# Kernel tuning notes

Measured on AMD Instinct MI355X. Metric: run time of the kernel, lower is better.

The kernel has to match this reference:

```python
import jax, jax.numpy as jnp
import numpy as np

D_MODEL = 1024
N_HEADS = 8
EDGE_HID = 512
N_EDGE_CLS = 18
N_NODE_CLS = 18
MAX_NODES = 15


def setup_inputs() -> dict:
    key = jax.random.key(0)
    ks = jax.random.split(key, 24)
    B, T, L, D = 32, 4, 1024, D_MODEL
    N = MAX_NODES
    s = 0.02
    visual_feats = jax.random.normal(ks[0], (B, T, L, D), jnp.float32)
    nodes = jax.random.randint(ks[1], (B, N), 0, N_NODE_CLS, dtype=jnp.int32)
    bboxes = jax.random.uniform(ks[2], (B, N, 4), jnp.float32)
    # embedding table; padding_idx=-1 -> last row zeroed (unused due to clamp)
    emb = (jax.random.normal(ks[3], (N_NODE_CLS + 1, D)) * s).at[-1].set(0.0)
    Wb = jax.random.normal(ks[4], (D, 4)) * s
    bb = jnp.zeros((D,), jnp.float32)
    Wq = jax.random.normal(ks[5], (D, D)) * s
    bq = jnp.zeros((D,), jnp.float32)
    Wk = jax.random.normal(ks[6], (D, D)) * s
    bk = jnp.zeros((D,), jnp.float32)
    Wv = jax.random.normal(ks[7], (D, D)) * s
    bv = jnp.zeros((D,), jnp.float32)
    Wo = jax.random.normal(ks[8], (D, D)) * s
    bo = jnp.zeros((D,), jnp.float32)
    W1 = jax.random.normal(ks[9], (EDGE_HID, 2 * D)) * s
    b1 = jnp.zeros((EDGE_HID,), jnp.float32)
    W2 = jax.random.normal(ks[10], (N_EDGE_CLS, EDGE_HID)) * s
    b2 = jnp.zeros((N_EDGE_CLS,), jnp.float32)
    Wh1 = jax.random.normal(ks[11], (256, D)) * s
    bh1 = jnp.zeros((256,), jnp.float32)
    Wh2 = jax.random.normal(ks[12], (1, 256)) * s
    bh2 = jnp.zeros((1,), jnp.float32)
    return dict(visual_feats=visual_feats, nodes=nodes, bboxes=bboxes, emb=emb,
                Wb=Wb, bb=bb, Wq=Wq, bq=bq, Wk=Wk, bk=bk, Wv=Wv, bv=bv,
                Wo=Wo, bo=bo, W1=W1, b1=b1, W2=W2, b2=b2,
                Wh1=Wh1, bh1=bh1, Wh2=Wh2, bh2=bh2)


def reference(visual_feats, nodes, bboxes, emb, Wb, bb, Wq, bq, Wk, bk, Wv, bv,
              Wo, bo, W1, b1, W2, b2, Wh1, bh1, Wh2, bh2):
    B, T, L, D = visual_feats.shape
    H = N_HEADS
    Hd = D // H
    v_f = visual_feats[:, -1]  # (B, L, D)
    n_emb = emb[jnp.maximum(nodes, 0)]            # (B, N, D)
    query = n_emb + bboxes @ Wb.T + bb            # (B, N, D)
    N = query.shape[1]
    # multi-head cross-attention (query=nodes, key/value=visual tokens)
    q = (query @ Wq.T + bq).reshape(B, N, H, Hd)
    k = (v_f @ Wk.T + bk).reshape(B, L, H, Hd)
    v = (v_f @ Wv.T + bv).reshape(B, L, H, Hd)
    scores = jnp.einsum('bnhd,blhd->bhnl', q, k) / jnp.sqrt(jnp.float32(Hd))
    attn = jax.nn.softmax(scores, axis=-1)
    ctx = jnp.einsum('bhnl,blhd->bnhd', attn, v).reshape(B, N, D)
    enriched = ctx @ Wo.T + bo                    # (B, N, D)
    pad = nodes == -1                             # all False here
    clean = jnp.where(pad[..., None], 0.0, enriched)
    # edge MLP: decompose first Linear over the concat into two half matmuls
    h_i = enriched @ W1[:, :D].T                  # (B, N, E)
    h_j = enriched @ W1[:, D:].T                  # (B, N, E)
    pair = jax.nn.relu(h_i[:, :, None, :] + h_j[:, None, :, :] + b1)  # (B,N,N,E)
    edge_logits = pair @ W2.T + b2                # (B, N, N, 18)
    valid = jnp.maximum(jnp.sum(~pad, axis=1, keepdims=True), 1).astype(enriched.dtype)
    gfeat = jnp.sum(clean, axis=1) / valid        # (B, D)
    energy = (jax.nn.relu(gfeat @ Wh1.T + bh1) @ Wh2.T + bh2).squeeze(-1)  # (B,)
    return edge_logits, energy
```

## Files before the change

### kernel.cpp

```cpp
#include <hip/hip_runtime.h>


typedef __attribute__((ext_vector_type(8))) short bf16x8;
typedef __attribute__((ext_vector_type(4))) float f32x4;

__device__ __forceinline__ unsigned short f2bf(float f) {
    unsigned int u = __float_as_uint(f);
    u = u + 0x7FFFu + ((u >> 16) & 1u);
    return (unsigned short)(u >> 16);
}

__device__ __forceinline__ void gload_lds16(const void* g, void* l) {
    __builtin_amdgcn_global_load_lds(
        (const __attribute__((address_space(1))) void*)g,
        (__attribute__((address_space(3))) void*)l,
        16, 0, 0);
}

__global__ __launch_bounds__(256) void bfgemm_k(
    const unsigned short* __restrict__ A, const unsigned short* __restrict__ B,
    unsigned short* __restrict__ C, int M, long sA, long sB, long sC)
{
    const int b  = blockIdx.z;
    const int m0 = blockIdx.y * 64;
    const int n0 = blockIdx.x * 128;
    const unsigned short* Ab = A + b * sA;
    const unsigned short* Bb = B + b * sB;

    __shared__ __align__(16) unsigned short As[64 * 32];
    __shared__ __align__(16) unsigned short Bs[128 * 32];

    const int t    = threadIdx.x;
    const int lane = t & 63;
    const int w    = t >> 6;
    const int wm   = w >> 1, wn = w & 1;

    f32x4 acc[2][4] = {};

    const int ar = t >> 2;
    const int ac = (t & 3) * 8;

    unsigned short* AsW  = As + w * 512;
    unsigned short* BsW0 = Bs + w * 512;
    unsigned short* BsW1 = Bs + 2048 + w * 512;
    const unsigned short* ga  = Ab + (long)(m0 + ar) * 1024 + ac;
    const unsigned short* gb0 = Bb + (long)(n0 + ar) * 1024 + ac;
    const unsigned short* gb1 = Bb + (long)(n0 + 64 + ar) * 1024 + ac;

    for (int k0 = 0; k0 < 1024; k0 += 32) {
        __syncthreads();
        gload_lds16(ga  + k0, AsW);
        gload_lds16(gb0 + k0, BsW0);
        gload_lds16(gb1 + k0, BsW1);
        __syncthreads();

        const int krow = (lane >> 4) * 8;
        bf16x8 af[2], bf[4];
#pragma unroll
        for (int fi = 0; fi < 2; ++fi)
            af[fi] = *(const bf16x8*)&As[(wm * 32 + fi * 16 + (lane & 15)) * 32 + krow];
#pragma unroll
        for (int fj = 0; fj < 4; ++fj)
            bf[fj] = *(const bf16x8*)&Bs[(wn * 64 + fj * 16 + (lane & 15)) * 32 + krow];
#pragma unroll
        for (int fi = 0; fi < 2; ++fi)
#pragma unroll
            for (int fj = 0; fj < 4; ++fj)
                acc[fi][fj] = __builtin_amdgcn_mfma_f32_16x16x32_bf16(
                    af[fi], bf[fj], acc[fi][fj], 0, 0, 0);
    }

    const int rbase = (lane >> 4) * 4;
    const int cn    = n0 + wn * 64 + (lane & 15);
#pragma unroll
    for (int fi = 0; fi < 2; ++fi) {
        const int mb = m0 + wm * 32 + fi * 16 + rbase;
#pragma unroll
        for (int r = 0; r < 4; ++r) {
            const int m = mb + r;
            if (m < M) {
#pragma unroll
                for (int fj = 0; fj < 4; ++fj)
                    C[b * sC + (long)m * 1024 + cn + fj * 16] = f2bf(acc[fi][fj][r]);
            }
        }
    }
}

__global__ __launch_bounds__(256) void sgemm_k(
    const unsigned short* __restrict__ A, const float* __restrict__ Bf,
    float* __restrict__ C, int M, long sA, long sB, long sC)
{
    const int b  = blockIdx.z;
    const int m0 = blockIdx.y * 64;
    const int n0 = blockIdx.x * 128;
    const unsigned short* Ab = A + b * sA;
    const float* Bb = Bf + b * sB;
    float* Cb = C + b * sC;

    __shared__ __align__(16) unsigned short As[64 * 32];
    __shared__ __align__(16) unsigned short Bs[128 * 32];

    const int t    = threadIdx.x;
    const int lane = t & 63;
    const int w    = t >> 6;
    const int wm   = w >> 1, wn = w & 1;

    f32x4 acc[2][4] = {};

    const int ar = t >> 2;
    const int ac = (t & 3) * 8;

    unsigned short* AsW = As + w * 512;
    const unsigned short* ga = Ab + (long)(m0 + ar) * 1024 + ac;
    const float* gb0 = Bb + (long)(n0 + ar) * 1024 + ac;
    const float* gb1 = Bb + (long)(n0 + 64 + ar) * 1024 + ac;

    for (int k0 = 0; k0 < 1024; k0 += 32) {
        float4 v0a = *(const float4*)(gb0 + k0);
        float4 v0b = *(const float4*)(gb0 + k0 + 4);
        float4 v1a = *(const float4*)(gb1 + k0);
        float4 v1b = *(const float4*)(gb1 + k0 + 4);
        __syncthreads();
        gload_lds16(ga + k0, AsW);
        ushort4 o;
        o.x = f2bf(v0a.x); o.y = f2bf(v0a.y); o.z = f2bf(v0a.z); o.w = f2bf(v0a.w);
        *(ushort4*)&Bs[t * 8] = o;
        o.x = f2bf(v0b.x); o.y = f2bf(v0b.y); o.z = f2bf(v0b.z); o.w = f2bf(v0b.w);
        *(ushort4*)&Bs[t * 8 + 4] = o;
        o.x = f2bf(v1a.x); o.y = f2bf(v1a.y); o.z = f2bf(v1a.z); o.w = f2bf(v1a.w);
        *(ushort4*)&Bs[2048 + t * 8] = o;
        o.x = f2bf(v1b.x); o.y = f2bf(v1b.y); o.z = f2bf(v1b.z); o.w = f2bf(v1b.w);
        *(ushort4*)&Bs[2048 + t * 8 + 4] = o;
        __syncthreads();

        const int krow = (lane >> 4) * 8;
        bf16x8 af[2], bf[4];
#pragma unroll
        for (int fi = 0; fi < 2; ++fi)
            af[fi] = *(const bf16x8*)&As[(wm * 32 + fi * 16 + (lane & 15)) * 32 + krow];
#pragma unroll
        for (int fj = 0; fj < 4; ++fj)
            bf[fj] = *(const bf16x8*)&Bs[(wn * 64 + fj * 16 + (lane & 15)) * 32 + krow];
#pragma unroll
        for (int fi = 0; fi < 2; ++fi)
#pragma unroll
            for (int fj = 0; fj < 4; ++fj)
                acc[fi][fj] = __builtin_amdgcn_mfma_f32_16x16x32_bf16(
                    af[fi], bf[fj], acc[fi][fj], 0, 0, 0);
    }

    const int rbase = (lane >> 4) * 4;
    const int cn    = n0 + wn * 64 + (lane & 15);
#pragma unroll
    for (int fi = 0; fi < 2; ++fi) {
        const int mb = m0 + wm * 32 + fi * 16 + rbase;
#pragma unroll
        for (int r = 0; r < 4; ++r) {
            const int m = mb + r;
            if (m < M) {
#pragma unroll
                for (int fj = 0; fj < 4; ++fj)
                    Cb[(long)m * 1024 + cn + fj * 16] = acc[fi][fj][r];
            }
        }
    }
}

template <int OM>
__global__ __launch_bounds__(256) void pgemm_k(
    const unsigned short* __restrict__ A, const unsigned short* __restrict__ B,
    const float* __restrict__ bias, float* __restrict__ C,
    unsigned short* __restrict__ Cbf,
    int M, int K, int lda, int ldb, int ldc)
{
    const int m0 = blockIdx.y * 64;
    const int n0 = blockIdx.x * 64;

    __shared__ __align__(16) unsigned short As[64 * 32];
    __shared__ __align__(16) unsigned short Bs[64 * 32];

    const int t    = threadIdx.x;
    const int lane = t & 63;
    const int w    = t >> 6;
    const int wm   = w >> 1, wn = w & 1;
    const int lm   = lane & 15, lg = lane >> 4;

    const int ar = t >> 2;
    const int ac = (t & 3) * 8;

    f32x4 acc[2][2] = {};

    unsigned short* AsW = As + w * 512;
    unsigned short* BsW = Bs + w * 512;
    const unsigned short* ga = A + (long)(m0 + ar) * lda + ac;
    const unsigned short* gb = B + (long)(n0 + ar) * ldb + ac;

    for (int k0 = 0; k0 < K; k0 += 32) {
        __syncthreads();
        gload_lds16(ga + k0, AsW);
        gload_lds16(gb + k0, BsW);
        __syncthreads();

        const int krow = lg * 8 & 24;
        bf16x8 af[2], bf[2];
#pragma unroll
        for (int fi = 0; fi < 2; ++fi)
            af[fi] = *(const bf16x8*)&As[(wm * 32 + fi * 16 + lm) * 32 + krow];
#pragma unroll
        for (int fj = 0; fj < 2; ++fj)
            bf[fj] = *(const bf16x8*)&Bs[(wn * 32 + fj * 16 + lm) * 32 + krow];
#pragma unroll
        for (int fi = 0; fi < 2; ++fi)
#pragma unroll
            for (int fj = 0; fj < 2; ++fj)
                acc[fi][fj] = __builtin_amdgcn_mfma_f32_16x16x32_bf16(
                    af[fi], bf[fj], acc[fi][fj], 0, 0, 0);
    }

    const int rbase = lg * 4;
#pragma unroll
    for (int fi = 0; fi < 2; ++fi) {
        const int mb = m0 + wm * 32 + fi * 16 + rbase;
#pragma unroll
        for (int r = 0; r < 4; ++r) {
            const int m = mb + r;
            if (m < M) {
#pragma unroll
                for (int fj = 0; fj < 2; ++fj) {
                    const int n = n0 + wn * 32 + fj * 16 + lm;
                    float v = acc[fi][fj][r];
                    if (bias) v += bias[n];
                    if constexpr (OM != 2) C[(long)m * ldc + n] = v;
                    if constexpr (OM >= 1) Cbf[(long)m * ldc + n] = f2bf(v);
                }
            }
        }
    }
}

__global__ __launch_bounds__(256) void qw_k(
    const unsigned short* __restrict__ qbf, const unsigned short* __restrict__ WkT,
    unsigned short* __restrict__ qW, float scale)
{
    const int z = blockIdx.y;
    const int b = z >> 3, h = z & 7;
    const int w = threadIdx.x >> 6, lane = threadIdx.x & 63;
    const int lm = lane & 15, lg = lane >> 4;
    const int n0w = blockIdx.x * 256 + w * 64;

    const unsigned short* Ar = qbf + (long)(b * 15 + lm) * 1024 + h * 128 + lg * 8;
    const unsigned short* Br = WkT + (long)(n0w + lm) * 1024 + h * 128 + lg * 8;

    bf16x8 af[4];
#pragma unroll
    for (int ks = 0; ks < 4; ++ks) af[ks] = *(const bf16x8*)(Ar + ks * 32);

    f32x4 acc[4] = {};
#pragma unroll
    for (int fj = 0; fj < 4; ++fj) {
#pragma unroll
        for (int ks = 0; ks < 4; ++ks) {
            bf16x8 bf = *(const bf16x8*)(Br + (long)fj * 16 * 1024 + ks * 32);
            acc[fj] = __builtin_amdgcn_mfma_f32_16x16x32_bf16(af[ks], bf, acc[fj], 0, 0, 0);
        }
    }

#pragma unroll
    for (int r = 0; r < 4; ++r) {
        const int m = lg * 4 + r;
        if (m < 15) {
#pragma unroll
            for (int fj = 0; fj < 4; ++fj)
                qW[(long)b * 131072 + (long)(m * 8 + h) * 1024 + n0w + fj * 16 + lm]
                    = f2bf(acc[fj][r] * scale);
        }
    }
}

__global__ __launch_bounds__(256) void ctx_k(
    const unsigned short* __restrict__ cf, const unsigned short* __restrict__ Wvb,
    const float* __restrict__ bv, unsigned short* __restrict__ ctx)
{
    const int z = blockIdx.x;
    const int b = z >> 3, h = z & 7;
    const int w = threadIdx.x >> 6, lane = threadIdx.x & 63;
    const int lm = lane & 15, lg = lane >> 4;

    const unsigned short* Ar = cf + (long)b * 122880 + (long)(lm * 8 + h) * 1024 + lg * 8;
    const unsigned short* Br = Wvb + (long)(h * 128 + w * 32 + lm) * 1024 + lg * 8;

    f32x4 acc[2] = {};
    for (int k0 = 0; k0 < 1024; k0 += 32) {
        bf16x8 af = *(const bf16x8*)(Ar + k0);
        bf16x8 b0 = *(const bf16x8*)(Br + k0);
        bf16x8 b1 = *(const bf16x8*)(Br + 16 * 1024 + k0);
        acc[0] = __builtin_amdgcn_mfma_f32_16x16x32_bf16(af, b0, acc[0], 0, 0, 0);
        acc[1] = __builtin_amdgcn_mfma_f32_16x16x32_bf16(af, b1, acc[1], 0, 0, 0);
    }

#pragma unroll
    for (int r = 0; r < 4; ++r) {
        const int m = lg * 4 + r;
        if (m < 15) {
#pragma unroll
            for (int fj = 0; fj < 2; ++fj) {
                const int gcol = h * 128 + w * 32 + fj * 16 + lm;
                ctx[(long)(b * 15 + m) * 1024 + gcol] = f2bf(acc[fj][r] + bv[gcol]);
            }
        }
    }
}

__global__ __launch_bounds__(256) void uber_cvt_k(
    const int* __restrict__ nodes, const float* __restrict__ bboxes,
    const float* __restrict__ emb, const float* __restrict__ Wb,
    const float* __restrict__ bb, unsigned short* __restrict__ qbf,
    const float* __restrict__ Wq, const float* __restrict__ Wo,
    const float* __restrict__ Wv, const float* __restrict__ W1,
    const float* __restrict__ Wk,
    unsigned short* __restrict__ dWq, unsigned short* __restrict__ dWo,
    unsigned short* __restrict__ dWv, unsigned short* __restrict__ dW1r,
    unsigned short* __restrict__ dWkT)
{
    __shared__ unsigned short tile[64][72];
    const int bid = blockIdx.x;
    const int t = threadIdx.x;

    if (bid < 4096) {
        const int which = bid >> 10;
        const int i = (bid & 1023) * 256 + t;
        const float* s;
        unsigned short* d;
        if (which == 3) {
            const int flat = i * 4, n = flat >> 10, k = flat & 1023;
            s = (n < 512) ? W1 + (long)n * 2048 + k
                          : W1 + (long)(n - 512) * 2048 + 1024 + k;
            d = dW1r + flat;
        } else {
            s = (which == 0 ? Wq : which == 1 ? Wo : Wv) + (long)i * 4;
            d = (which == 0 ? dWq : which == 1 ? dWo : dWv) + (long)i * 4;
        }
        float4 v = *(const float4*)s;
        ushort4 o;
        o.x = f2bf(v.x); o.y = f2bf(v.y); o.z = f2bf(v.z); o.w = f2bf(v.w);
        *(ushort4*)d = o;
    } else if (bid < 4352) {
        const int tl = bid - 4096;
        const int d0 = (tl >> 4) * 64, e0 = (tl & 15) * 64;
        const int r0 = t >> 4, c0 = (t & 15) * 4;
#pragma unroll
        for (int rr = 0; rr < 4; ++rr) {
            const int r = r0 + rr * 16;
            float4 v = *(const float4*)&Wk[(long)(d0 + r) * 1024 + e0 + c0];
            tile[r][c0 + 0] = f2bf(v.x); tile[r][c0 + 1] = f2bf(v.y);
            tile[r][c0 + 2] = f2bf(v.z); tile[r][c0 + 3] = f2bf(v.w);
        }
        __syncthreads();
#pragma unroll
        for (int rr = 0; rr < 4; ++rr) {
            const int idx = rr * 256 + t;
            const int e = idx >> 4, c4 = (idx & 15) * 4;
            ushort4 o;
            o.x = tile[c4 + 0][e]; o.y = tile[c4 + 1][e];
            o.z = tile[c4 + 2][e]; o.w = tile[c4 + 3][e];
            *(ushort4*)&dWkT[(long)(e0 + e) * 1024 + d0 + c4] = o;
        }
    } else {
        const int blk = bid - 4352;
        const int node = nodes[blk];
        const int idx = node < 0 ? 0 : node;
        const float4 bx = *(const float4*)&bboxes[blk * 4];
        const float* er = emb + (long)idx * 1024;
        for (int d = t; d < 1024; d += 256) {
            const float4 w = *(const float4*)&Wb[d * 4];
            qbf[(long)blk * 1024 + d] = f2bf(
                er[d] + bb[d] + bx.x * w.x + bx.y * w.y + bx.z * w.z + bx.w * w.w);
        }
    }
}

__global__ __launch_bounds__(256) void cvtT_k(
    const float* __restrict__ vf, unsigned short* __restrict__ vbfT)
{
    const int b  = blockIdx.z;
    const int e0 = blockIdx.x * 64;
    const int l0 = blockIdx.y * 64;
    const float* src = vf + (long)b * 4194304;
    __shared__ unsigned short tile[64][72];
    const int t = threadIdx.x;
    const int r0 = t >> 4, c0 = (t & 15) * 4;
#pragma unroll
    for (int rr = 0; rr < 4; ++rr) {
        const int r = r0 + rr * 16;
        float4 v = *(const float4*)&src[(long)(l0 + r) * 1024 + e0 + c0];
        tile[r][c0 + 0] = f2bf(v.x); tile[r][c0 + 1] = f2bf(v.y);
        tile[r][c0 + 2] = f2bf(v.z); tile[r][c0 + 3] = f2bf(v.w);
    }
    __syncthreads();
#pragma unroll
    for (int rr = 0; rr < 4; ++rr) {
        const int idx = rr * 256 + t;
        const int e   = idx >> 4;
        const int c4  = (idx & 15) * 4;
        ushort4 o;
        o.x = tile[c4 + 0][e]; o.y = tile[c4 + 1][e];
        o.z = tile[c4 + 2][e]; o.w = tile[c4 + 3][e];
        *(ushort4*)&vbfT[(long)b * 1048576 + (long)(e0 + e) * 1024 + l0 + c4] = o;
    }
}

__global__ __launch_bounds__(256) void softmax_k(
    const float* __restrict__ sc, unsigned short* __restrict__ attn)
{
    __shared__ float red[4];
    const int blk = blockIdx.x;
    const int b = blk / 120, r = blk % 120;
    const float* p = sc + (long)blk * 1024;
    const int t = threadIdx.x;
    float4 v = *(const float4*)&p[t * 4];

    float m = fmaxf(fmaxf(v.x, v.y), fmaxf(v.z, v.w));
#pragma unroll
    for (int o = 32; o; o >>= 1) m = fmaxf(m, __shfl_xor(m, o));
    if ((t & 63) == 0) red[t >> 6] = m;
    __syncthreads();
    m = fmaxf(fmaxf(red[0], red[1]), fmaxf(red[2], red[3]));
    __syncthreads();

    v.x = __expf(v.x - m); v.y = __expf(v.y - m);
    v.z = __expf(v.z - m); v.w = __expf(v.w - m);
    float s = v.x + v.y + v.z + v.w;
#pragma unroll
    for (int o = 32; o; o >>= 1) s += __shfl_xor(s, o);
    if ((t & 63) == 0) red[t >> 6] = s;
    __syncthreads();
    s = red[0] + red[1] + red[2] + red[3];
    const float inv = 1.0f / s;
    ushort4 o;
    o.x = f2bf(v.x * inv); o.y = f2bf(v.y * inv);
    o.z = f2bf(v.z * inv); o.w = f2bf(v.w * inv);
    *(ushort4*)&attn[(long)(b * 128 + r) * 1024 + t * 4] = o;
}

__global__ __launch_bounds__(320) void tail_k(
    const float* __restrict__ hh, const float* __restrict__ b1,
    const float* __restrict__ W2, const float* __restrict__ b2,
    const float* __restrict__ enr, const int* __restrict__ nodes,
    const float* __restrict__ Wh1, const float* __restrict__ bh1,
    const float* __restrict__ Wh2, float* __restrict__ hidr,
    float* __restrict__ out)
{
    __shared__ float sm[8993];
    const int bid = blockIdx.x;
    const int t = threadIdx.x;

    if (bid < 480) {
        const int b = bid / 15, i = bid % 15;
        float* hiS = sm;
        float* b1S = sm + 256;
        float* hjS = sm + 512;
        float* w2S = sm + 512 + 3855;
        const int j = t / 18, c = t % 18;
        float acc = 0.0f;

        for (int u0 = 0; u0 < 512; u0 += 256) {
            __syncthreads();
            if (t < 64) {
                float4 v = *(const float4*)&hh[(long)(b * 15 + i) * 1024 + u0 + t * 4];
                hiS[t * 4 + 0] = v.x; hiS[t * 4 + 1] = v.y;
                hiS[t * 4 + 2] = v.z; hiS[t * 4 + 3] = v.w;
            } else if (t < 128) {
                const int tt = t - 64;
                float4 v = *(const float4*)&b1[u0 + tt * 4];
                b1S[tt * 4 + 0] = v.x; b1S[tt * 4 + 1] = v.y;
                b1S[tt * 4 + 2] = v.z; b1S[tt * 4 + 3] = v.w;
            }
            for (int x = t; x < 960; x += 320) {
                const int r = x >> 6, cc = (x & 63) * 4;
                float4 v = *(const float4*)&hh[(long)(b * 15 + r) * 1024 + 512 + u0 + cc];
                hjS[r * 257 + cc + 0] = v.x; hjS[r * 257 + cc + 1] = v.y;
                hjS[r * 257 + cc + 2] = v.z; hjS[r * 257 + cc + 3] = v.w;
            }
            for (int x = t; x < 1152; x += 320) {
                const int r = x >> 6, cc = (x & 63) * 4;
                float4 v = *(const float4*)&W2[(long)r * 512 + u0 + cc];
                w2S[r * 257 + cc + 0] = v.x; w2S[r * 257 + cc + 1] = v.y;
                w2S[r * 257 + cc + 2] = v.z; w2S[r * 257 + cc + 3] = v.w;
            }
            __syncthreads();
            if (t < 270) {
                for (int u = 0; u < 256; ++u) {
                    float p = hiS[u] + hjS[j * 257 + u] + b1S[u];
                    p = p > 0.0f ? p : 0.0f;
                    acc += p * w2S[c * 257 + u];
                }
            }
        }
        if (t < 270)
            out[((long)(bid) * 15 + j) * 18 + c] = acc + b2[c];
    } else {
        const int z = bid - 480;
        const int u0 = (z & 15) * 16;
        const int b  = z >> 4;
        float* gf = sm;

        int cnt = 0;
#pragma unroll
        for (int n = 0; n < 15; ++n) cnt += (nodes[b * 15 + n] != -1) ? 1 : 0;
        const float inv_valid = 1.0f / fmaxf((float)cnt, 1.0f);
        if (t < 256) {
            for (int e = t; e < 1024; e += 256) {
                float s = 0.0f;
#pragma unroll
                for (int n = 0; n < 15; ++n) {
                    const bool ok = nodes[b * 15 + n] != -1;
                    s += ok ? enr[(long)(b * 15 + n) * 1024 + e] : 0.0f;
                }
                gf[e] = s * inv_valid;
            }
        }
        __syncthreads();
        if (t < 256) {
            const int wave = t >> 6, lane = t & 63;
#pragma unroll
            for (int r = 0; r < 4; ++r) {
                const int u = u0 + wave * 4 + r;
                float s = 0.0f;
#pragma unroll
                for (int e0 = 0; e0 < 1024; e0 += 64)
                    s += gf[e0 + lane] * Wh1[(long)u * 1024 + e0 + lane];
#pragma unroll
                for (int o = 32; o; o >>= 1) s += __shfl_xor(s, o);
                if (lane == 0)
                    hidr[b * 256 + u] = fmaxf(s + bh1[u], 0.0f) * Wh2[u];
            }
        }
    }
}

__global__ __launch_bounds__(256) void energy3_k(
    const float* __restrict__ hidr, const float* __restrict__ bh2,
    float* __restrict__ out)
{
    const int b = blockIdx.x;
    const int t = threadIdx.x;
    __shared__ float red[4];
    float v = hidr[b * 256 + t];
#pragma unroll
    for (int o = 32; o; o >>= 1) v += __shfl_xor(v, o);
    if ((t & 63) == 0) red[t >> 6] = v;
    __syncthreads();
    if (t == 0) out[129600 + b] = red[0] + red[1] + red[2] + red[3] + bh2[0];
}

extern "C" void kernel_launch(void* const* d_in, const int* in_sizes, int n_in,
                              void* d_out, int out_size, void* d_ws, size_t ws_size,
                              hipStream_t stream)
{
    const float* visual = (const float*)d_in[0];
    const int*   nodes  = (const int*)  d_in[1];
    const float* bboxes = (const float*)d_in[2];
    const float* emb    = (const float*)d_in[3];
    const float* Wb     = (const float*)d_in[4];
    const float* bb     = (const float*)d_in[5];
    const float* Wq     = (const float*)d_in[6];
    const float* bq     = (const float*)d_in[7];
    const float* Wk     = (const float*)d_in[8];
    const float* Wv     = (const float*)d_in[10];
    const float* bv     = (const float*)d_in[11];
    const float* Wo     = (const float*)d_in[12];
    const float* bo     = (const float*)d_in[13];
    const float* W1     = (const float*)d_in[14];
    const float* b1     = (const float*)d_in[15];
    const float* W2     = (const float*)d_in[16];
    const float* b2     = (const float*)d_in[17];
    const float* Wh1    = (const float*)d_in[18];
    const float* bh1    = (const float*)d_in[19];
    const float* Wh2    = (const float*)d_in[20];
    const float* bh2    = (const float*)d_in[21];

    float* out = (float*)d_out;
    float* ws  = (float*)d_ws;

    unsigned short* query_bf = (unsigned short*)(ws);
    unsigned short* q_bf     = (unsigned short*)(ws + 131072);
    float* scores = ws + 262144;
    unsigned short* ctxf_bf  = (unsigned short*)(ws + 4194304);
    unsigned short* ctx_bf   = (unsigned short*)(ws + 6160384);
    float* enr    = ws + 6422528;
    unsigned short* enr_bf   = (unsigned short*)(ws + 6914048);
    float* hh     = ws + 7176192;
    unsigned short* Wq_bf  = (unsigned short*)(ws + 7667712);
    unsigned short* Wo_bf  = (unsigned short*)(ws + 8192000);
    unsigned short* Wv_bf  = (unsigned short*)(ws + 8716288);
    unsigned short* W1r_bf = (unsigned short*)(ws + 9240576);
    unsigned short* WkT_bf = (unsigned short*)(ws + 9764864);
    unsigned short* qW_bf   = (unsigned short*)(ws + 10289152);
    unsigned short* attn_bf = (unsigned short*)(ws + 12386304);
    unsigned short* v_bfT   = (unsigned short*)(ws + 31260672);
    float* hidr   = ws + 48070656;

    const float inv_sqrt_hd = 0.08838834764831845f;
    const float* v_f = visual + 3 * 1048576;

    uber_cvt_k<<<4832, 256, 0, stream>>>(
        nodes, bboxes, emb, Wb, bb, query_bf,
        Wq, Wo, Wv, W1, Wk, Wq_bf, Wo_bf, Wv_bf, W1r_bf, WkT_bf);

    pgemm_k<2><<<dim3(16, 8), 256, 0, stream>>>(
        query_bf, Wq_bf, bq, nullptr, q_bf, 480, 1024, 1024, 1024, 1024);

    qw_k<<<dim3(4, 256), 256, 0, stream>>>(q_bf, WkT_bf, qW_bf, inv_sqrt_hd);

    sgemm_k<<<dim3(8, 2, 32), 256, 0, stream>>>(
        qW_bf, v_f, scores, 120, 131072, 4194304, 122880);

    cvtT_k<<<dim3(16, 16, 32), 256, 0, stream>>>(v_f, v_bfT);

    softmax_k<<<3840, 256, 0, stream>>>(scores, attn_bf);

    bfgemm_k<<<dim3(8, 2, 32), 256, 0, stream>>>(
        attn_bf, v_bfT, ctxf_bf, 120, 131072, 1048576, 122880);

    ctx_k<<<256, 256, 0, stream>>>(ctxf_bf, Wv_bf, bv, ctx_bf);

    pgemm_k<1><<<dim3(16, 8), 256, 0, stream>>>(
        ctx_bf, Wo_bf, bo, enr, enr_bf, 480, 1024, 1024, 1024, 1024);

    pgemm_k<0><<<dim3(16, 8), 256, 0, stream>>>(
        enr_bf, W1r_bf, nullptr, hh, nullptr, 480, 1024, 1024, 1024, 1024);

    tail_k<<<992, 320, 0, stream>>>(
        hh, b1, W2, b2, enr, nodes, Wh1, bh1, Wh2, hidr, out);

    energy3_k<<<32, 256, 0, stream>>>(hidr, bh2, out);
}
```

Before: 215.9 us.

## Merge score GEMM with V transpose-convert, fold energy reduction into tail

The scores GEMM (sgemm) and the bf16 transpose-conversion of the visual features (cvtT) now run as a single launch, with blocks split by block index and sharing one LDS buffer. The energy head is moved into tail_k: each of 32 blocks computes all 256 hidden units and the final reduction, which removes the energy3 launch and the hidr workspace round trip. Together this drops two kernel launches and lets the two independent reads of v_f overlap. The cost is that the energy part now has only 32 blocks each doing 16x the work serially, where there were 512 blocks before, which could lengthen the tail kernel's critical path.

```diff
diff --git a/kernel.cpp b/kernel.cpp
--- a/kernel.cpp
+++ b/kernel.cpp
@@ -87,82 +87,113 @@
     }
 }
 
-__global__ __launch_bounds__(256) void sgemm_k(
-    const unsigned short* __restrict__ A, const float* __restrict__ Bf,
-    float* __restrict__ C, int M, long sA, long sB, long sC)
-{
-    const int b  = blockIdx.z;
-    const int m0 = blockIdx.y * 64;
-    const int n0 = blockIdx.x * 128;
-    const unsigned short* Ab = A + b * sA;
-    const float* Bb = Bf + b * sB;
-    float* Cb = C + b * sC;
-
-    __shared__ __align__(16) unsigned short As[64 * 32];
-    __shared__ __align__(16) unsigned short Bs[128 * 32];
-
-    const int t    = threadIdx.x;
-    const int lane = t & 63;
-    const int w    = t >> 6;
-    const int wm   = w >> 1, wn = w & 1;
-
-    f32x4 acc[2][4] = {};
-
-    const int ar = t >> 2;
-    const int ac = (t & 3) * 8;
-
-    unsigned short* AsW = As + w * 512;
-    const unsigned short* ga = Ab + (long)(m0 + ar) * 1024 + ac;
-    const float* gb0 = Bb + (long)(n0 + ar) * 1024 + ac;
-    const float* gb1 = Bb + (long)(n0 + 64 + ar) * 1024 + ac;
-
-    for (int k0 = 0; k0 < 1024; k0 += 32) {
-        float4 v0a = *(const float4*)(gb0 + k0);
-        float4 v0b = *(const float4*)(gb0 + k0 + 4);
-        float4 v1a = *(const float4*)(gb1 + k0);
-        float4 v1b = *(const float4*)(gb1 + k0 + 4);
-        __syncthreads();
-        gload_lds16(ga + k0, AsW);
-        ushort4 o;
-        o.x = f2bf(v0a.x); o.y = f2bf(v0a.y); o.z = f2bf(v0a.z); o.w = f2bf(v0a.w);
-        *(ushort4*)&Bs[t * 8] = o;
-        o.x = f2bf(v0b.x); o.y = f2bf(v0b.y); o.z = f2bf(v0b.z); o.w = f2bf(v0b.w);
-        *(ushort4*)&Bs[t * 8 + 4] = o;
-        o.x = f2bf(v1a.x); o.y = f2bf(v1a.y); o.z = f2bf(v1a.z); o.w = f2bf(v1a.w);
-        *(ushort4*)&Bs[2048 + t * 8] = o;
-        o.x = f2bf(v1b.x); o.y = f2bf(v1b.y); o.z = f2bf(v1b.z); o.w = f2bf(v1b.w);
-        *(ushort4*)&Bs[2048 + t * 8 + 4] = o;
-        __syncthreads();
-
-        const int krow = (lane >> 4) * 8;
-        bf16x8 af[2], bf[4];
-#pragma unroll
-        for (int fi = 0; fi < 2; ++fi)
-            af[fi] = *(const bf16x8*)&As[(wm * 32 + fi * 16 + (lane & 15)) * 32 + krow];
-#pragma unroll
-        for (int fj = 0; fj < 4; ++fj)
-            bf[fj] = *(const bf16x8*)&Bs[(wn * 64 + fj * 16 + (lane & 15)) * 32 + krow];
-#pragma unroll
-        for (int fi = 0; fi < 2; ++fi)
+__global__ __launch_bounds__(256) void sv_k(
+    const unsigned short* __restrict__ A, const float* __restrict__ vf,
+    float* __restrict__ C, unsigned short* __restrict__ vbfT, int M)
+{
+    __shared__ __align__(16) unsigned short sm_u[6144];
+    const int bid = blockIdx.x;
+    const int t = threadIdx.x;
+
+    if (bid < 512) {
+        const int b  = bid >> 4;
+        const int m0 = ((bid >> 3) & 1) * 64;
+        const int n0 = (bid & 7) * 128;
+        const unsigned short* Ab = A + (long)b * 131072;
+        const float* Bb = vf + (long)b * 4194304;
+        float* Cb = C + (long)b * 122880;
+
+        unsigned short* As = sm_u;
+        unsigned short* Bs = sm_u + 2048;
+
+        const int lane = t & 63;
+        const int w    = t >> 6;
+        const int wm   = w >> 1, wn = w & 1;
+
+        f32x4 acc[2][4] = {};
+
+        const int ar = t >> 2;
+        const int ac = (t & 3) * 8;
+
+        unsigned short* AsW = As + w * 512;
+        const unsigned short* ga = Ab + (long)(m0 + ar) * 1024 + ac;
+        const float* gb0 = Bb + (long)(n0 + ar) * 1024 + ac;
+        const float* gb1 = Bb + (long)(n0 + 64 + ar) * 1024 + ac;
+
+        for (int k0 = 0; k0 < 1024; k0 += 32) {
+            float4 v0a = *(const float4*)(gb0 + k0);
+            float4 v0b = *(const float4*)(gb0 + k0 + 4);
+            float4 v1a = *(const float4*)(gb1 + k0);
+            float4 v1b = *(const float4*)(gb1 + k0 + 4);
+            __syncthreads();
+            gload_lds16(ga + k0, AsW);
+            ushort4 o;
+            o.x = f2bf(v0a.x); o.y = f2bf(v0a.y); o.z = f2bf(v0a.z); o.w = f2bf(v0a.w);
+            *(ushort4*)&Bs[t * 8] = o;
+            o.x = f2bf(v0b.x); o.y = f2bf(v0b.y); o.z = f2bf(v0b.z); o.w = f2bf(v0b.w);
+            *(ushort4*)&Bs[t * 8 + 4] = o;
+            o.x = f2bf(v1a.x); o.y = f2bf(v1a.y); o.z = f2bf(v1a.z); o.w = f2bf(v1a.w);
+            *(ushort4*)&Bs[2048 + t * 8] = o;
+            o.x = f2bf(v1b.x); o.y = f2bf(v1b.y); o.z = f2bf(v1b.z); o.w = f2bf(v1b.w);
+            *(ushort4*)&Bs[2048 + t * 8 + 4] = o;
+            __syncthreads();
+
+            const int krow = (lane >> 4) * 8;
+            bf16x8 af[2], bf[4];
+#pragma unroll
+            for (int fi = 0; fi < 2; ++fi)
+                af[fi] = *(const bf16x8*)&As[(wm * 32 + fi * 16 + (lane & 15)) * 32 + krow];
 #pragma unroll
             for (int fj = 0; fj < 4; ++fj)
-                acc[fi][fj] = __builtin_amdgcn_mfma_f32_16x16x32_bf16(
-                    af[fi], bf[fj], acc[fi][fj], 0, 0, 0);
-    }
-
-    const int rbase = (lane >> 4) * 4;
-    const int cn    = n0 + wn * 64 + (lane & 15);
-#pragma unroll
-    for (int fi = 0; fi < 2; ++fi) {
-        const int mb = m0 + wm * 32 + fi * 16 + rbase;
-#pragma unroll
-        for (int r = 0; r < 4; ++r) {
-            const int m = mb + r;
-            if (m < M) {
+                bf[fj] = *(const bf16x8*)&Bs[(wn * 64 + fj * 16 + (lane & 15)) * 32 + krow];
+#pragma unroll
+            for (int fi = 0; fi < 2; ++fi)
 #pragma unroll
                 for (int fj = 0; fj < 4; ++fj)
-                    Cb[(long)m * 1024 + cn + fj * 16] = acc[fi][fj][r];
-            }
+                    acc[fi][fj] = __builtin_amdgcn_mfma_f32_16x16x32_bf16(
+                        af[fi], bf[fj], acc[fi][fj], 0, 0, 0);
+        }
+
+        const int rbase = (lane >> 4) * 4;
+        const int cn    = n0 + wn * 64 + (lane & 15);
+#pragma unroll
+        for (int fi = 0; fi < 2; ++fi) {
+            const int mb = m0 + wm * 32 + fi * 16 + rbase;
+#pragma unroll
+            for (int r = 0; r < 4; ++r) {
+                const int m = mb + r;
+                if (m < M) {
+#pragma unroll
+                    for (int fj = 0; fj < 4; ++fj)
+                        Cb[(long)m * 1024 + cn + fj * 16] = acc[fi][fj][r];
+                }
+            }
+        }
+    } else {
+        const int tl = bid - 512;
+        const int b  = tl >> 8;
+        const int e0 = (tl & 15) * 64;
+        const int l0 = ((tl >> 4) & 15) * 64;
+        const float* src = vf + (long)b * 4194304;
+        unsigned short* tile = sm_u;
+        const int r0 = t >> 4, c0 = (t & 15) * 4;
+#pragma unroll
+        for (int rr = 0; rr < 4; ++rr) {
+            const int r = r0 + rr * 16;
+            float4 v = *(const float4*)&src[(long)(l0 + r) * 1024 + e0 + c0];
+            tile[r * 72 + c0 + 0] = f2bf(v.x); tile[r * 72 + c0 + 1] = f2bf(v.y);
+            tile[r * 72 + c0 + 2] = f2bf(v.z); tile[r * 72 + c0 + 3] = f2bf(v.w);
+        }
+        __syncthreads();
+#pragma unroll
+        for (int rr = 0; rr < 4; ++rr) {
+            const int idx = rr * 256 + t;
+            const int e   = idx >> 4;
+            const int c4  = (idx & 15) * 4;
+            ushort4 o;
+            o.x = tile[(c4 + 0) * 72 + e]; o.y = tile[(c4 + 1) * 72 + e];
+            o.z = tile[(c4 + 2) * 72 + e]; o.w = tile[(c4 + 3) * 72 + e];
+            *(ushort4*)&vbfT[(long)b * 1048576 + (long)(e0 + e) * 1024 + l0 + c4] = o;
         }
     }
 }
@@ -380,36 +411,6 @@
     }
 }
 
-__global__ __launch_bounds__(256) void cvtT_k(
-    const float* __restrict__ vf, unsigned short* __restrict__ vbfT)
-{
-    const int b  = blockIdx.z;
-    const int e0 = blockIdx.x * 64;
-    const int l0 = blockIdx.y * 64;
-    const float* src = vf + (long)b * 4194304;
-    __shared__ unsigned short tile[64][72];
-    const int t = threadIdx.x;
-    const int r0 = t >> 4, c0 = (t & 15) * 4;
-#pragma unroll
-    for (int rr = 0; rr < 4; ++rr) {
-        const int r = r0 + rr * 16;
-        float4 v = *(const float4*)&src[(long)(l0 + r) * 1024 + e0 + c0];
-        tile[r][c0 + 0] = f2bf(v.x); tile[r][c0 + 1] = f2bf(v.y);
-        tile[r][c0 + 2] = f2bf(v.z); tile[r][c0 + 3] = f2bf(v.w);
-    }
-    __syncthreads();
-#pragma unroll
-    for (int rr = 0; rr < 4; ++rr) {
-        const int idx = rr * 256 + t;
-        const int e   = idx >> 4;
-        const int c4  = (idx & 15) * 4;
-        ushort4 o;
-        o.x = tile[c4 + 0][e]; o.y = tile[c4 + 1][e];
-        o.z = tile[c4 + 2][e]; o.w = tile[c4 + 3][e];
-        *(ushort4*)&vbfT[(long)b * 1048576 + (long)(e0 + e) * 1024 + l0 + c4] = o;
-    }
-}
-
 __global__ __launch_bounds__(256) void softmax_k(
     const float* __restrict__ sc, unsigned short* __restrict__ attn)
 {
@@ -448,7 +449,7 @@
     const float* __restrict__ W2, const float* __restrict__ b2,
     const float* __restrict__ enr, const int* __restrict__ nodes,
     const float* __restrict__ Wh1, const float* __restrict__ bh1,
-    const float* __restrict__ Wh2, float* __restrict__ hidr,
+    const float* __restrict__ Wh2, const float* __restrict__ bh2,
     float* __restrict__ out)
 {
     __shared__ float sm[8993];
@@ -500,10 +501,10 @@
         if (t < 270)
             out[((long)(bid) * 15 + j) * 18 + c] = acc + b2[c];
     } else {
-        const int z = bid - 480;
-        const int u0 = (z & 15) * 16;
-        const int b  = z >> 4;
-        float* gf = sm;
+        const int b = bid - 480;
+        float* gf  = sm;
+        float* hid = sm + 1024;
+        float* red = sm + 1280;
 
         int cnt = 0;
 #pragma unroll
@@ -523,35 +524,31 @@
         __syncthreads();
         if (t < 256) {
             const int wave = t >> 6, lane = t & 63;
-#pragma unroll
-            for (int r = 0; r < 4; ++r) {
-                const int u = u0 + wave * 4 + r;
-                float s = 0.0f;
-#pragma unroll
-                for (int e0 = 0; e0 < 1024; e0 += 64)
-                    s += gf[e0 + lane] * Wh1[(long)u * 1024 + e0 + lane];
-#pragma unroll
-                for (int o = 32; o; o >>= 1) s += __shfl_xor(s, o);
-                if (lane == 0)
-                    hidr[b * 256 + u] = fmaxf(s + bh1[u], 0.0f) * Wh2[u];
-            }
-        }
-    }
-}
-
-__global__ __launch_bounds__(256) void energy3_k(
-    const float* __restrict__ hidr, const float* __restrict__ bh2,
-    float* __restrict__ out)
-{
-    const int b = blockIdx.x;
-    const int t = threadIdx.x;
-    __shared__ float red[4];
-    float v = hidr[b * 256 + t];
-#pragma unroll
-    for (int o = 32; o; o >>= 1) v += __shfl_xor(v, o);
-    if ((t & 63) == 0) red[t >> 6] = v;
-    __syncthreads();
-    if (t == 0) out[129600 + b] = red[0] + red[1] + red[2] + red[3] + bh2[0];
+            for (int c16 = 0; c16 < 256; c16 += 16) {
+#pragma unroll
+                for (int r = 0; r < 4; ++r) {
+                    const int u = c16 + wave * 4 + r;
+                    float s = 0.0f;
+#pragma unroll
+                    for (int e0 = 0; e0 < 1024; e0 += 64)
+                        s += gf[e0 + lane] * Wh1[(long)u * 1024 + e0 + lane];
+#pragma unroll
+                    for (int o = 32; o; o >>= 1) s += __shfl_xor(s, o);
+                    if (lane == 0)
+                        hid[u] = fmaxf(s + bh1[u], 0.0f) * Wh2[u];
+                }
+            }
+        }
+        __syncthreads();
+        if (t < 256) {
+            float v = hid[t];
+#pragma unroll
+            for (int o = 32; o; o >>= 1) v += __shfl_xor(v, o);
+            if ((t & 63) == 0) red[t >> 6] = v;
+        }
+        __syncthreads();
+        if (t == 0) out[129600 + b] = red[0] + red[1] + red[2] + red[3] + bh2[0];
+    }
 }
 
 extern "C" void kernel_launch(void* const* d_in, const int* in_sizes, int n_in,
@@ -599,7 +596,6 @@
     unsigned short* qW_bf   = (unsigned short*)(ws + 10289152);
     unsigned short* attn_bf = (unsigned short*)(ws + 12386304);
     unsigned short* v_bfT   = (unsigned short*)(ws + 31260672);
-    float* hidr   = ws + 48070656;
 
     const float inv_sqrt_hd = 0.08838834764831845f;
     const float* v_f = visual + 3 * 1048576;
@@ -613,10 +609,7 @@
 
     qw_k<<<dim3(4, 256), 256, 0, stream>>>(q_bf, WkT_bf, qW_bf, inv_sqrt_hd);
 
-    sgemm_k<<<dim3(8, 2, 32), 256, 0, stream>>>(
-        qW_bf, v_f, scores, 120, 131072, 4194304, 122880);
-
-    cvtT_k<<<dim3(16, 16, 32), 256, 0, stream>>>(v_f, v_bfT);
+    sv_k<<<8704, 256, 0, stream>>>(qW_bf, v_f, scores, v_bfT, 120);
 
     softmax_k<<<3840, 256, 0, stream>>>(scores, attn_bf);
 
@@ -631,8 +624,6 @@
     pgemm_k<0><<<dim3(16, 8), 256, 0, stream>>>(
         enr_bf, W1r_bf, nullptr, hh, nullptr, 480, 1024, 1024, 1024, 1024);
 
-    tail_k<<<992, 320, 0, stream>>>(
-        hh, b1, W2, b2, enr, nodes, Wh1, bh1, Wh2, hidr, out);
-
-    energy3_k<<<32, 256, 0, stream>>>(hidr, bh2, out);
-}
+    tail_k<<<512, 320, 0, stream>>>(
+        hh, b1, W2, b2, enr, nodes, Wh1, bh1, Wh2, bh2, out);
+}
```

Result: slower. 240.6 us (+11.5%).
